# Performance work log

Measured on AMD Instinct MI355X. Metric: run time of the kernel, lower is better.

The kernel has to match this reference:

```python
import jax, jax.numpy as jnp
import numpy as np

NH = 16   # num_heads
HD = 128  # head_dim
HS = 2048 # hidden_size
LI, LT = 2048, 512
MLP = 4 * HS


def _ln(x, s, b):
    m = jnp.mean(x, axis=-1, keepdims=True)
    v = jnp.var(x, axis=-1, keepdims=True)
    return (x - m) * jax.lax.rsqrt(v + 1e-6) * s + b


def _rms(x, s):
    return x * jax.lax.rsqrt(jnp.mean(x * x, axis=-1, keepdims=True) + 1e-6) * s


def _mod6(vec, w, b):
    a = (jax.nn.silu(vec) @ w + b)[:, None, :]
    return jnp.split(a, 6, axis=-1)  # shift1,scale1,gate1,shift2,scale2,gate2


def _rope(x, pe):
    B, H, L, D = x.shape
    xr = x.reshape(B, H, L, D // 2, 1, 2)
    return (pe[..., 0] * xr[..., 0] + pe[..., 1] * xr[..., 1]).reshape(B, H, L, D)


def _attention(q, k, v, pe):
    q = _rope(q, pe)
    k = _rope(k, pe)
    scores = jnp.einsum('bhqd,bhkd->bhqk', q, k) * (q.shape[-1] ** -0.5)
    p = jax.nn.softmax(scores, axis=-1)
    o = jnp.einsum('bhqk,bhkd->bhqd', p, v)
    B, H, L, D = o.shape
    return o.transpose(0, 2, 1, 3).reshape(B, L, H * D)


def _prenorm_qkv(x, shift, scale, ln_s, ln_b, qkv_w, qkv_b, qn, kn):
    xm = (1.0 + scale) * _ln(x, ln_s, ln_b) + shift
    y = xm @ qkv_w + qkv_b
    B, L, _ = y.shape
    y = y.reshape(B, L, 3, NH, HD).transpose(2, 0, 3, 1, 4)  # K B H L D
    q, k, v = y[0], y[1], y[2]
    return _rms(q, qn), _rms(k, kn), v


def _forward(img, txt, vec, pe,
             img_mod_w, img_mod_b, img_norm1_s, img_norm1_b, img_qkv_w, img_qkv_b,
             img_qn_s, img_kn_s, img_proj_w, img_proj_b, img_norm2_s, img_norm2_b,
             img_mlp_w1, img_mlp_b1, img_mlp_w2, img_mlp_b2,
             txt_mod_w, txt_mod_b, txt_norm1_s, txt_norm1_b, txt_qkv_w, txt_qkv_b,
             txt_qn_s, txt_kn_s, txt_proj_w, txt_proj_b, txt_norm2_s, txt_norm2_b,
             txt_mlp_w1, txt_mlp_b1, txt_mlp_w2, txt_mlp_b2):
    i_sh1, i_sc1, i_g1, i_sh2, i_sc2, i_g2 = _mod6(vec, img_mod_w, img_mod_b)
    t_sh1, t_sc1, t_g1, t_sh2, t_sc2, t_g2 = _mod6(vec, txt_mod_w, txt_mod_b)

    iq, ik, iv = _prenorm_qkv(img, i_sh1, i_sc1, img_norm1_s, img_norm1_b,
                              img_qkv_w, img_qkv_b, img_qn_s, img_kn_s)
    tq, tk, tv = _prenorm_qkv(txt, t_sh1, t_sc1, txt_norm1_s, txt_norm1_b,
                              txt_qkv_w, txt_qkv_b, txt_qn_s, txt_kn_s)

    q = jnp.concatenate((tq, iq), axis=2)
    k = jnp.concatenate((tk, ik), axis=2)
    v = jnp.concatenate((tv, iv), axis=2)
    attn = _attention(q, k, v, pe)  # [B, LT+LI, HS]
    Lt = txt.shape[1]
    txt_attn, img_attn = attn[:, :Lt], attn[:, Lt:]

    img = img + i_g1 * (img_attn @ img_proj_w + img_proj_b)
    img_h = (1.0 + i_sc2) * _ln(img, img_norm2_s, img_norm2_b) + i_sh2
    img = img + i_g2 * (jax.nn.gelu(img_h @ img_mlp_w1 + img_mlp_b1) @ img_mlp_w2 + img_mlp_b2)

    txt = txt + t_g1 * (txt_attn @ txt_proj_w + txt_proj_b)
    txt_h = (1.0 + t_sc2) * _ln(txt, txt_norm2_s, txt_norm2_b) + t_sh2
    txt = txt + t_g2 * (jax.nn.gelu(txt_h @ txt_mlp_w1 + txt_mlp_b1) @ txt_mlp_w2 + txt_mlp_b2)
    return img, txt


def setup_inputs() -> dict:
    key = jax.random.key(0)
    ki = iter(jax.random.split(key, 48))
    def n(shape, s=0.02):
        return jax.random.normal(next(ki), shape, jnp.float32) * s
    d = {
        'img': jax.random.normal(next(ki), (1, LI, HS), jnp.float32),
        'txt': jax.random.normal(next(ki), (1, LT, HS), jnp.float32),
        'vec': jax.random.normal(next(ki), (1, HS), jnp.float32),
        'pe': jax.random.normal(next(ki), (1, 1, LT + LI, HD // 2, 2, 2), jnp.float32),
    }
    for p in ('img', 'txt'):
        d[p + '_mod_w'] = n((HS, 6 * HS)); d[p + '_mod_b'] = jnp.zeros((6 * HS,), jnp.float32)
        d[p + '_norm1_s'] = jnp.ones((HS,), jnp.float32); d[p + '_norm1_b'] = jnp.zeros((HS,), jnp.float32)
        d[p + '_qkv_w'] = n((HS, 3 * HS)); d[p + '_qkv_b'] = jnp.zeros((3 * HS,), jnp.float32)
        d[p + '_qn_s'] = jnp.ones((HD,), jnp.float32); d[p + '_kn_s'] = jnp.ones((HD,), jnp.float32)
        d[p + '_proj_w'] = n((HS, HS)); d[p + '_proj_b'] = jnp.zeros((HS,), jnp.float32)
        d[p + '_norm2_s'] = jnp.ones((HS,), jnp.float32); d[p + '_norm2_b'] = jnp.zeros((HS,), jnp.float32)
        d[p + '_mlp_w1'] = n((HS, MLP)); d[p + '_mlp_b1'] = jnp.zeros((MLP,), jnp.float32)
        d[p + '_mlp_w2'] = n((MLP, HS)); d[p + '_mlp_b2'] = jnp.zeros((HS,), jnp.float32)
    return d


def reference(img, txt, vec, pe,
              img_mod_w, img_mod_b, img_norm1_s, img_norm1_b, img_qkv_w, img_qkv_b,
              img_qn_s, img_kn_s, img_proj_w, img_proj_b, img_norm2_s, img_norm2_b,
              img_mlp_w1, img_mlp_b1, img_mlp_w2, img_mlp_b2,
              txt_mod_w, txt_mod_b, txt_norm1_s, txt_norm1_b, txt_qkv_w, txt_qkv_b,
              txt_qn_s, txt_kn_s, txt_proj_w, txt_proj_b, txt_norm2_s, txt_norm2_b,
              txt_mlp_w1, txt_mlp_b1, txt_mlp_w2, txt_mlp_b2):
    return _forward(img, txt, vec, pe,
                    img_mod_w, img_mod_b, img_norm1_s, img_norm1_b, img_qkv_w, img_qkv_b,
                    img_qn_s, img_kn_s, img_proj_w, img_proj_b, img_norm2_s, img_norm2_b,
                    img_mlp_w1, img_mlp_b1, img_mlp_w2, img_mlp_b2,
                    txt_mod_w, txt_mod_b, txt_norm1_s, txt_norm1_b, txt_qkv_w, txt_qkv_b,
                    txt_qn_s, txt_kn_s, txt_proj_w, txt_proj_b, txt_norm2_s, txt_norm2_b,
                    txt_mlp_w1, txt_mlp_b1, txt_mlp_w2, txt_mlp_b2)
```

## Files before the change

### kernel.cpp

```cpp
#include <hip/hip_runtime.h>
#include <hip/hip_bf16.h>
#include <math.h>

typedef __bf16 bf16;
typedef __bf16 bf16x2 __attribute__((ext_vector_type(2)));
typedef __bf16 bf16x8 __attribute__((ext_vector_type(8)));
typedef float f32x4 __attribute__((ext_vector_type(4)));

#define HS 2048
#define NH 16
#define HD 128
#define LT 512
#define LI 2048
#define LQ 2560
#define MLP_D 8192
#define SPLIT 4
#define KVS (LQ / SPLIT)
#define KVBLK 32
#define NTILES (KVS / KVBLK)

__device__ __forceinline__ f32x4 mfma16(bf16x8 a, bf16x8 b, f32x4 c) {
  return __builtin_amdgcn_mfma_f32_16x16x32_bf16(a, b, c, 0, 0, 0);
}

__device__ __forceinline__ void gl_lds16(const bf16* g, bf16* l) {
  __builtin_amdgcn_global_load_lds((const __attribute__((address_space(1))) void*)g,
                                   (__attribute__((address_space(3))) void*)l, 16, 0, 0);
}

__global__ void k_silu(const float* __restrict__ v, float* __restrict__ s) {
  int i = blockIdx.x * 256 + threadIdx.x;
  float x = v[i];
  s[i] = x / (1.f + expf(-x));
}

__global__ __launch_bounds__(256) void k_mod_partial(
    const float* __restrict__ s, const float* __restrict__ w_txt,
    const float* __restrict__ w_img, float* __restrict__ part) {
  int strm = blockIdx.x / 48;
  int n = (blockIdx.x % 48) * 256 + threadIdx.x;
  const float* w = strm ? w_img : w_txt;
  int k0 = blockIdx.y * 256;
  __shared__ float sl[256];
  sl[threadIdx.x] = s[k0 + threadIdx.x];
  __syncthreads();
  float acc = 0.f;
  for (int k = 0; k < 256; k++)
    acc += sl[k] * w[(size_t)(k0 + k) * 12288 + n];
  part[((size_t)blockIdx.y * 2 + strm) * 12288 + n] = acc;
}

__global__ __launch_bounds__(256) void k_mod_reduce(
    const float* __restrict__ part, const float* __restrict__ b_txt,
    const float* __restrict__ b_img, float* __restrict__ mod) {
  int strm = blockIdx.x / 48;
  int n = (blockIdx.x % 48) * 256 + threadIdx.x;
  float acc = strm ? b_img[n] : b_txt[n];
  for (int kc = 0; kc < 8; kc++)
    acc += part[((size_t)kc * 2 + strm) * 12288 + n];
  mod[(size_t)strm * 12288 + n] = acc;
}

__global__ __launch_bounds__(256) void k_transpose_cvt(
    const float* __restrict__ src, bf16* __restrict__ dst, int R, int C) {
  __shared__ float t[64][65];
  int tx = threadIdx.x & 63, ty = threadIdx.x >> 6;
  int c0 = blockIdx.x * 64, r0 = blockIdx.y * 64;
  for (int i = 0; i < 64; i += 4)
    t[ty + i][tx] = src[(size_t)(r0 + ty + i) * C + c0 + tx];
  __syncthreads();
#pragma unroll
  for (int j = 0; j < 2; j++) {
    int c = (threadIdx.x >> 3) + j * 32;
    int gg = (threadIdx.x & 7) * 8;
    bf16x8 ov;
#pragma unroll
    for (int k = 0; k < 8; k++) ov[k] = (bf16)t[gg + k][c];
    *(bf16x8*)(dst + (size_t)(c0 + c) * R + r0 + gg) = ov;
  }
}

__global__ __launch_bounds__(256) void k_ln_mod(
    const float* __restrict__ x0, const float* __restrict__ x1,
    const float* __restrict__ ls0, const float* __restrict__ lb0,
    const float* __restrict__ ls1, const float* __restrict__ lb1,
    const float* __restrict__ mod0, const float* __restrict__ mod1,
    int shidx, int scidx, bf16* __restrict__ out) {
  int r = blockIdx.x;
  int strm = r >= LT;
  const float* x = strm ? (x1 + (size_t)(r - LT) * HS) : (x0 + (size_t)r * HS);
  const float* ls = strm ? ls1 : ls0;
  const float* lb = strm ? lb1 : lb0;
  const float* md = strm ? mod1 : mod0;
  const float* sh = md + (size_t)shidx * HS;
  const float* sc = md + (size_t)scidx * HS;
  int t = threadIdx.x;
  float4 a = ((const float4*)x)[t * 2];
  float4 b = ((const float4*)x)[t * 2 + 1];
  float xv[8] = {a.x, a.y, a.z, a.w, b.x, b.y, b.z, b.w};
  float sum = 0.f, sq = 0.f;
#pragma unroll
  for (int j = 0; j < 8; j++) { sum += xv[j]; sq += xv[j] * xv[j]; }
#pragma unroll
  for (int m = 32; m; m >>= 1) { sum += __shfl_xor(sum, m); sq += __shfl_xor(sq, m); }
  __shared__ float red[8];
  int lane = t & 63, wid = t >> 6;
  if (!lane) { red[wid] = sum; red[wid + 4] = sq; }
  __syncthreads();
  float ts = red[0] + red[1] + red[2] + red[3];
  float tq = red[4] + red[5] + red[6] + red[7];
  float mean = ts * (1.f / HS);
  float var = tq * (1.f / HS) - mean * mean;
  float inv = rsqrtf(var + 1e-6f);
  int c0 = t * 8;
  bf16x8 ov;
#pragma unroll
  for (int j = 0; j < 8; j++) {
    int c = c0 + j;
    float v = ((xv[j] - mean) * inv * ls[c] + lb[c]) * (1.f + sc[c]) + sh[c];
    ov[j] = (bf16)v;
  }
  *(bf16x8*)(out + (size_t)r * HS + c0) = ov;
}

template <int MODE>
__global__ __launch_bounds__(256) void k_gemm(
    const bf16* __restrict__ A, int K, int N, int Ksz,
    const bf16* __restrict__ BT0, const bf16* __restrict__ BT1,
    const float* __restrict__ bias0, const float* __restrict__ bias1,
    void* __restrict__ out0, void* __restrict__ out1) {
  __shared__ bf16 As[128 * 32];
  __shared__ bf16 Bs[128 * 32];
  int tid = threadIdx.x;
  int bn = blockIdx.x, bm = blockIdx.y;
  int strm = (bm * 128) >= LT;
  int lm = bm * 128 - strm * LT;
  const bf16* BT = strm ? BT1 : BT0;
  int lane = tid & 63, wid = tid >> 6;
  int wr = wid >> 1, wc = wid & 1;
  int sr = tid >> 2, sc8 = (tid & 3) * 8;
  const bf16* Ag = A + (size_t)(bm * 128 + sr) * K + sc8;
  const bf16* Bg = BT + (size_t)(bn * 128 + sr) * K + sc8;
  bf16* As_dst = As + wid * 512;
  bf16* Bs_dst = Bs + wid * 512;
  int kbeg = MODE == 4 ? blockIdx.z * Ksz : 0;
  f32x4 acc[4][4] = {};
  for (int k0 = kbeg; k0 < kbeg + Ksz; k0 += 32) {
    __syncthreads();
    gl_lds16(Ag + k0, As_dst);
    gl_lds16(Ag + (size_t)64 * K + k0, As_dst + 2048);
    gl_lds16(Bg + k0, Bs_dst);
    gl_lds16(Bg + (size_t)64 * K + k0, Bs_dst + 2048);
    __syncthreads();
    bf16x8 af[4], bfr[4];
    int r16 = lane & 15, kc8 = (lane >> 4) * 8;
#pragma unroll
    for (int m = 0; m < 4; m++) af[m] = *(const bf16x8*)&As[(wr * 64 + m * 16 + r16) * 32 + kc8];
#pragma unroll
    for (int n = 0; n < 4; n++) bfr[n] = *(const bf16x8*)&Bs[(wc * 64 + n * 16 + r16) * 32 + kc8];
#pragma unroll
    for (int m = 0; m < 4; m++)
#pragma unroll
      for (int n = 0; n < 4; n++)
        acc[m][n] = mfma16(af[m], bfr[n], acc[m][n]);
  }
  int col = lane & 15, rb = (lane >> 4) * 4;
  const float* bias = strm ? bias1 : bias0;
  float* part = MODE == 4 ? (float*)out0 + (size_t)blockIdx.z * LQ * N : nullptr;
#pragma unroll
  for (int m = 0; m < 4; m++) {
#pragma unroll
    for (int n = 0; n < 4; n++) {
      int gn = bn * 128 + wc * 64 + n * 16 + col;
      float bv = MODE == 4 ? 0.f : bias[gn];
#pragma unroll
      for (int r = 0; r < 4; r++) {
        int lr = wr * 64 + m * 16 + rb + r;
        float v = acc[m][n][r] + bv;
        if (MODE == 0) {
          ((bf16*)(strm ? out1 : out0))[(size_t)(lm + lr) * N + gn] = (bf16)v;
        } else if (MODE == 2) {
          float g = 0.5f * v * (1.f + tanhf(0.7978845608028654f * (v + 0.044715f * v * v * v)));
          ((bf16*)(strm ? out1 : out0))[(size_t)(lm + lr) * N + gn] = (bf16)g;
        } else {
          part[(size_t)(bm * 128 + lr) * N + gn] = v;
        }
      }
    }
  }
}

template <int S>
__global__ __launch_bounds__(256) void k_skcomb(
    const float* __restrict__ part, int N,
    const float* __restrict__ bias0, const float* __restrict__ bias1,
    const float* __restrict__ gate0, const float* __restrict__ gate1,
    const float* __restrict__ res0, const float* __restrict__ res1,
    float* __restrict__ out0, float* __restrict__ out1) {
  int gid = blockIdx.x * 256 + threadIdx.x;
  int nv = N >> 2;
  int row = gid / nv, cv = gid - row * nv;
  int strm = row >= LT;
  int lrow = row - strm * LT;
  const float* bias = strm ? bias1 : bias0;
  const float* gate = strm ? gate1 : gate0;
  const float* res = strm ? res1 : res0;
  float* out = strm ? out1 : out0;
  int c = cv * 4;
  float4 acc = *(const float4*)(bias + c);
#pragma unroll
  for (int s = 0; s < S; s++) {
    float4 p = *(const float4*)(part + ((size_t)s * LQ + row) * N + c);
    acc.x += p.x; acc.y += p.y; acc.z += p.z; acc.w += p.w;
  }
  float4 g = *(const float4*)(gate + c);
  float4 r = *(const float4*)(res + (size_t)lrow * N + c);
  float4 o = {r.x + g.x * acc.x, r.y + g.y * acc.y, r.z + g.z * acc.z, r.w + g.w * acc.w};
  *(float4*)(out + (size_t)lrow * N + c) = o;
}

__global__ __launch_bounds__(256) void k_qkv_post(
    const bf16* __restrict__ y, const float* __restrict__ pe,
    const float* __restrict__ qn0, const float* __restrict__ kn0,
    const float* __restrict__ qn1, const float* __restrict__ kn1,
    bf16* __restrict__ qh, bf16* __restrict__ kh) {
  int wv = (int)((blockIdx.x * 256 + threadIdx.x) >> 6);
  int lane = threadIdx.x & 63;
  int head = wv / LQ, l = wv - head * LQ;
  const bf16* yr = y + (size_t)l * (3 * HS) + head * HD;
  float q0 = (float)yr[2 * lane], q1 = (float)yr[2 * lane + 1];
  float k0 = (float)yr[HS + 2 * lane], k1 = (float)yr[HS + 2 * lane + 1];
  float sqs = q0 * q0 + q1 * q1, sks = k0 * k0 + k1 * k1;
#pragma unroll
  for (int m = 1; m < 64; m <<= 1) { sqs += __shfl_xor(sqs, m); sks += __shfl_xor(sks, m); }
  float rq = rsqrtf(sqs * (1.f / HD) + 1e-6f);
  float rk = rsqrtf(sks * (1.f / HD) + 1e-6f);
  int strm = l >= LT;
  const float* qn = strm ? qn1 : qn0;
  const float* kn = strm ? kn1 : kn0;
  float e0 = q0 * rq * qn[2 * lane], e1 = q1 * rq * qn[2 * lane + 1];
  float f0 = k0 * rk * kn[2 * lane], f1 = k1 * rk * kn[2 * lane + 1];
  float4 p = *(const float4*)(pe + ((size_t)l * 64 + lane) * 4);
  const float scl = 0.08838834764831845f;
  size_t qi = ((size_t)head * LQ + l) * HD + 2 * lane;
  bf16x2 qv = {(bf16)((p.x * e0 + p.y * e1) * scl), (bf16)((p.z * e0 + p.w * e1) * scl)};
  bf16x2 kv = {(bf16)(p.x * f0 + p.y * f1), (bf16)(p.z * f0 + p.w * f1)};
  *(bf16x2*)(qh + qi) = qv;
  *(bf16x2*)(kh + qi) = kv;
}

__global__ __launch_bounds__(256) void k_vtrans(const bf16* __restrict__ y,
                                                bf16* __restrict__ vT) {
  __shared__ bf16 t[32][34];
  int head = blockIdx.y >> 2, dt = blockIdx.y & 3;
  int tx = threadIdx.x & 31, ty = threadIdx.x >> 5;
  int l0 = blockIdx.x * 32, d0 = dt * 32;
  for (int i = 0; i < 32; i += 8)
    t[ty + i][tx] = y[(size_t)(l0 + ty + i) * (3 * HS) + 2 * HS + head * HD + d0 + tx];
  __syncthreads();
  for (int i = 0; i < 32; i += 8)
    vT[(size_t)(head * HD + d0 + ty + i) * LQ + l0 + tx] = t[tx][ty + i];
}

__global__ __launch_bounds__(256, 4) void k_attn(
    const bf16* __restrict__ Q, const bf16* __restrict__ Kh,
    const bf16* __restrict__ VT, bf16* __restrict__ Op, float* __restrict__ ml) {
  __shared__ bf16 Ks[2][KVBLK * 128];
  __shared__ bf16 Vs[2][128 * KVBLK];
  __shared__ bf16 P[4][16 * 34];
  int tid = threadIdx.x, lane = tid & 63, w = tid >> 6;
  int b = blockIdx.x;
  int qb = b % 40;
  int split = (b / 40) % SPLIT;
  int head = b / (40 * SPLIT);
  int qr = qb * 64 + w * 16;
  int r16 = lane & 15, g = lane >> 4;
  const bf16* qp = Q + ((size_t)head * LQ + qr + r16) * HD + g * 8;
  bf16x8 qf[4];
#pragma unroll
  for (int c = 0; c < 4; c++) qf[c] = *(const bf16x8*)(qp + c * 32);
  f32x4 O[8] = {};
  float mr[4], lr[4];
#pragma unroll
  for (int i = 0; i < 4; i++) { mr[i] = -1e30f; lr[i] = 0.f; }
  bf16* pl = &P[w][0];
  const bf16* kbase = Kh + ((size_t)head * LQ + split * KVS) * HD;
  const bf16* vbase = VT + (size_t)head * HD * LQ + split * KVS;
  int krow0 = w * 8 + (lane >> 4);
  int kslot = lane & 15;
  int vrow0 = w * 32 + (lane >> 2);
  int vslot = lane & 3;
  auto stage = [&](int buf, int t) {
    int kv0 = t * KVBLK;
#pragma unroll
    for (int i = 0; i < 2; i++) {
      int krow = krow0 + i * 4;
      gl_lds16(kbase + (size_t)(kv0 + krow) * HD + ((kslot ^ (krow & 7)) << 3),
               &Ks[buf][(w * 8 + i * 4) * 128]);
      int vrow = vrow0 + i * 16;
      gl_lds16(vbase + (size_t)vrow * LQ + kv0 + ((vslot ^ (vrow & 3)) << 3),
               &Vs[buf][(w * 32 + i * 16) * KVBLK]);
    }
  };
  stage(0, 0);
  int cur = 0;
  for (int t = 0; t < NTILES; t++) {
    __syncthreads();
    if (t + 1 < NTILES) stage(cur ^ 1, t + 1);
    const bf16* ks = &Ks[cur][0];
    const bf16* vs = &Vs[cur][0];
    f32x4 S0 = {}, S1 = {};
    int sw = (r16 & 7);
#pragma unroll
    for (int c = 0; c < 4; c++) {
      int slot = ((4 * c + g) ^ sw) << 3;
      bf16x8 ka = *(const bf16x8*)&ks[r16 * 128 + slot];
      bf16x8 kb = *(const bf16x8*)&ks[(16 + r16) * 128 + slot];
      S0 = mfma16(qf[c], ka, S0);
      S1 = mfma16(qf[c], kb, S1);
    }
    float alpha[4];
#pragma unroll
    for (int i = 0; i < 4; i++) {
      float mx = fmaxf(S0[i], S1[i]);
#pragma unroll
      for (int m = 8; m; m >>= 1) mx = fmaxf(mx, __shfl_xor(mx, m));
      float mn = fmaxf(mr[i], mx);
      float p0 = __expf(S0[i] - mn), p1 = __expf(S1[i] - mn);
      float rs = p0 + p1;
#pragma unroll
      for (int m = 8; m; m >>= 1) rs += __shfl_xor(rs, m);
      alpha[i] = __expf(mr[i] - mn);
      lr[i] = lr[i] * alpha[i] + rs;
      mr[i] = mn;
      pl[(4 * g + i) * 34 + r16] = (bf16)p0;
      pl[(4 * g + i) * 34 + 16 + r16] = (bf16)p1;
    }
    bf16x8 pf = *(const bf16x8*)&pl[r16 * 34 + g * 8];
    int vsl = (g ^ (r16 & 3)) * 8;
#pragma unroll
    for (int n = 0; n < 8; n++) {
      f32x4 o = O[n];
#pragma unroll
      for (int i = 0; i < 4; i++) o[i] *= alpha[i];
      bf16x8 vf = *(const bf16x8*)&vs[(n * 16 + r16) * KVBLK + vsl];
      O[n] = mfma16(pf, vf, o);
    }
    cur ^= 1;
  }
  const int NL = NH * LQ;
  bf16* op = Op + (size_t)split * NL * HD;
#pragma unroll
  for (int n = 0; n < 8; n++)
#pragma unroll
    for (int i = 0; i < 4; i++)
      op[((size_t)head * LQ + qr + 4 * g + i) * HD + n * 16 + r16] = (bf16)O[n][i];
  if (r16 == 0) {
#pragma unroll
    for (int i = 0; i < 4; i++) {
      int idx = head * LQ + qr + 4 * g + i;
      ml[(size_t)(split * 2 + 0) * NL + idx] = mr[i];
      ml[(size_t)(split * 2 + 1) * NL + idx] = lr[i];
    }
  }
}

__global__ __launch_bounds__(256) void k_attn_combine(
    const bf16* __restrict__ Op, const float* __restrict__ ml, bf16* __restrict__ out) {
  int lane = threadIdx.x & 63, w = threadIdx.x >> 6;
  int row = blockIdx.x * 4 + w;
  int head = row / LQ, l = row - head * LQ;
  const int NL = NH * LQ;
  float ms[SPLIT], ls[SPLIT], m = -1e30f;
#pragma unroll
  for (int s = 0; s < SPLIT; s++) {
    ms[s] = ml[(size_t)(s * 2) * NL + row];
    ls[s] = ml[(size_t)(s * 2 + 1) * NL + row];
    m = fmaxf(m, ms[s]);
  }
  float wsum = 0.f, wgt[SPLIT];
#pragma unroll
  for (int s = 0; s < SPLIT; s++) { wgt[s] = __expf(ms[s] - m); wsum += wgt[s] * ls[s]; }
  float inv = 1.f / wsum;
  size_t oi = (size_t)row * HD + 2 * lane;
  float a0 = 0.f, a1 = 0.f;
#pragma unroll
  for (int s = 0; s < SPLIT; s++) {
    bf16x2 v = *(const bf16x2*)(Op + (size_t)s * NL * HD + oi);
    a0 += wgt[s] * (float)v[0];
    a1 += wgt[s] * (float)v[1];
  }
  bf16x2 ov = {(bf16)(a0 * inv), (bf16)(a1 * inv)};
  *(bf16x2*)(out + (size_t)l * HS + head * HD + 2 * lane) = ov;
}

extern "C" void kernel_launch(void* const* d_in, const int* in_sizes, int n_in,
                              void* d_out, int out_size, void* d_ws, size_t ws_size,
                              hipStream_t stream) {
  const float* img = (const float*)d_in[0];
  const float* txt = (const float*)d_in[1];
  const float* vec = (const float*)d_in[2];
  const float* pe = (const float*)d_in[3];
#define PARAM(i) ((const float*)d_in[i])

  char* ws = (char*)d_ws;
  size_t off = 0;
  auto alloc = [&](size_t b) { void* p = ws + off; off += (b + 255) & ~(size_t)255; return p; };
  float* silu_s = (float*)alloc((size_t)HS * 4);
  float* mpart = (float*)alloc((size_t)8 * 2 * 12288 * 4);
  float* mod = (float*)alloc((size_t)2 * 6 * HS * 4);
  bf16* qkvT0 = (bf16*)alloc((size_t)3 * HS * HS * 2);
  bf16* qkvT1 = (bf16*)alloc((size_t)3 * HS * HS * 2);
  bf16* projT0 = (bf16*)alloc((size_t)HS * HS * 2);
  bf16* projT1 = (bf16*)alloc((size_t)HS * HS * 2);
  bf16* mlp1T0 = (bf16*)alloc((size_t)MLP_D * HS * 2);
  bf16* mlp1T1 = (bf16*)alloc((size_t)MLP_D * HS * 2);
  bf16* mlp2T0 = (bf16*)alloc((size_t)HS * MLP_D * 2);
  bf16* mlp2T1 = (bf16*)alloc((size_t)HS * MLP_D * 2);
  bf16* xm = (bf16*)alloc((size_t)LQ * HS * 2);
  bf16* y = (bf16*)alloc((size_t)LQ * 3 * HS * 2);
  bf16* qh = (bf16*)alloc((size_t)NH * LQ * HD * 2);
  bf16* kh = (bf16*)alloc((size_t)NH * LQ * HD * 2);
  bf16* vT = (bf16*)alloc((size_t)NH * HD * LQ * 2);
  bf16* attnb = (bf16*)alloc((size_t)LQ * HS * 2);
  float* x2 = (float*)alloc((size_t)LQ * HS * 4);
  bf16* xm2 = (bf16*)alloc((size_t)LQ * HS * 2);
  bf16* h = (bf16*)alloc((size_t)LQ * MLP_D * 2);
  float* ml = (float*)alloc((size_t)2 * SPLIT * NH * LQ * 4);
  bf16* Op = h;
  float* skpart = (float*)xm;
  (void)ws_size; (void)in_sizes; (void)n_in; (void)out_size;

  const float* t_mod = mod;
  const float* i_mod = mod + 6 * HS;

  k_silu<<<HS / 256, 256, 0, stream>>>(vec, silu_s);
  k_mod_partial<<<dim3(96, 8), 256, 0, stream>>>(silu_s, PARAM(20), PARAM(4), mpart);
  k_mod_reduce<<<96, 256, 0, stream>>>(mpart, PARAM(21), PARAM(5), mod);

  k_transpose_cvt<<<dim3(3 * HS / 64, HS / 64), 256, 0, stream>>>(PARAM(24), qkvT0, HS, 3 * HS);
  k_transpose_cvt<<<dim3(3 * HS / 64, HS / 64), 256, 0, stream>>>(PARAM(8), qkvT1, HS, 3 * HS);
  k_transpose_cvt<<<dim3(HS / 64, HS / 64), 256, 0, stream>>>(PARAM(28), projT0, HS, HS);
  k_transpose_cvt<<<dim3(HS / 64, HS / 64), 256, 0, stream>>>(PARAM(12), projT1, HS, HS);
  k_transpose_cvt<<<dim3(MLP_D / 64, HS / 64), 256, 0, stream>>>(PARAM(32), mlp1T0, HS, MLP_D);
  k_transpose_cvt<<<dim3(MLP_D / 64, HS / 64), 256, 0, stream>>>(PARAM(16), mlp1T1, HS, MLP_D);
  k_transpose_cvt<<<dim3(HS / 64, MLP_D / 64), 256, 0, stream>>>(PARAM(34), mlp2T0, MLP_D, HS);
  k_transpose_cvt<<<dim3(HS / 64, MLP_D / 64), 256, 0, stream>>>(PARAM(18), mlp2T1, MLP_D, HS);

  k_ln_mod<<<LQ, 256, 0, stream>>>(txt, img, PARAM(22), PARAM(23), PARAM(6), PARAM(7),
                                   t_mod, i_mod, 0, 1, xm);

  k_gemm<0><<<dim3(3 * HS / 128, LQ / 128), 256, 0, stream>>>(
      xm, HS, 3 * HS, HS, qkvT0, qkvT1, PARAM(25), PARAM(9), y, y + (size_t)LT * 3 * HS);

  k_qkv_post<<<NH * LQ / 4, 256, 0, stream>>>(y, pe, PARAM(26), PARAM(27), PARAM(10), PARAM(11),
                                              qh, kh);
  k_vtrans<<<dim3(LQ / 32, NH * 4), 256, 0, stream>>>(y, vT);

  k_attn<<<NH * SPLIT * 40, 256, 0, stream>>>(qh, kh, vT, Op, ml);
  k_attn_combine<<<NH * LQ / 4, 256, 0, stream>>>(Op, ml, attnb);

  k_gemm<4><<<dim3(HS / 128, LQ / 128, 2), 256, 0, stream>>>(
      attnb, HS, HS, HS / 2, projT0, projT1, nullptr, nullptr, skpart, nullptr);
  k_skcomb<2><<<LQ * HS / 4 / 256, 256, 0, stream>>>(
      skpart, HS, PARAM(29), PARAM(13), t_mod + 2 * HS, i_mod + 2 * HS, txt, img,
      x2, x2 + (size_t)LT * HS);

  k_ln_mod<<<LQ, 256, 0, stream>>>(x2, x2 + (size_t)LT * HS, PARAM(30), PARAM(31), PARAM(14),
                                   PARAM(15), t_mod, i_mod, 3, 4, xm2);

  k_gemm<2><<<dim3(MLP_D / 128, LQ / 128), 256, 0, stream>>>(
      xm2, HS, MLP_D, HS, mlp1T0, mlp1T1, PARAM(33), PARAM(17), h, h + (size_t)LT * MLP_D);

  float* out_img = (float*)d_out;
  float* out_txt = (float*)d_out + (size_t)LI * HS;
  k_gemm<4><<<dim3(HS / 128, LQ / 128, 4), 256, 0, stream>>>(
      h, MLP_D, HS, MLP_D / 4, mlp2T0, mlp2T1, nullptr, nullptr, skpart, nullptr);
  k_skcomb<4><<<LQ * HS / 4 / 256, 256, 0, stream>>>(
      skpart, HS, PARAM(35), PARAM(19), t_mod + 5 * HS, i_mod + 5 * HS, x2,
      x2 + (size_t)LT * HS, out_txt, out_img);
}
```

Before: 860.4 us.

## Double-buffer GEMM LDS tiles, XOR-swizzle shared layout, use exp-based GELU

```diff
diff --git a/kernel.cpp b/kernel.cpp
--- a/kernel.cpp
+++ b/kernel.cpp
@@ -129,8 +129,8 @@
     const bf16* __restrict__ BT0, const bf16* __restrict__ BT1,
     const float* __restrict__ bias0, const float* __restrict__ bias1,
     void* __restrict__ out0, void* __restrict__ out1) {
-  __shared__ bf16 As[128 * 32];
-  __shared__ bf16 Bs[128 * 32];
+  __shared__ bf16 As[2][128 * 32];
+  __shared__ bf16 Bs[2][128 * 32];
   int tid = threadIdx.x;
   int bn = blockIdx.x, bm = blockIdx.y;
   int strm = (bm * 128) >= LT;
@@ -138,31 +138,40 @@
   const bf16* BT = strm ? BT1 : BT0;
   int lane = tid & 63, wid = tid >> 6;
   int wr = wid >> 1, wc = wid & 1;
-  int sr = tid >> 2, sc8 = (tid & 3) * 8;
-  const bf16* Ag = A + (size_t)(bm * 128 + sr) * K + sc8;
-  const bf16* Bg = BT + (size_t)(bn * 128 + sr) * K + sc8;
-  bf16* As_dst = As + wid * 512;
-  bf16* Bs_dst = Bs + wid * 512;
+  int sr = tid >> 2;
+  int scol = ((tid & 3) ^ (sr & 3)) * 8;
+  const bf16* Ag = A + (size_t)(bm * 128 + sr) * K + scol;
+  const bf16* Bg = BT + (size_t)(bn * 128 + sr) * K + scol;
   int kbeg = MODE == 4 ? blockIdx.z * Ksz : 0;
+  int nk = Ksz / 32;
+  auto stage = [&](int buf, int ks) {
+    int k0 = kbeg + ks * 32;
+    gl_lds16(Ag + k0, &As[buf][wid * 512]);
+    gl_lds16(Ag + (size_t)64 * K + k0, &As[buf][2048 + wid * 512]);
+    gl_lds16(Bg + k0, &Bs[buf][wid * 512]);
+    gl_lds16(Bg + (size_t)64 * K + k0, &Bs[buf][2048 + wid * 512]);
+  };
   f32x4 acc[4][4] = {};
-  for (int k0 = kbeg; k0 < kbeg + Ksz; k0 += 32) {
+  int r16 = lane & 15, g = lane >> 4;
+  int fslot = (g ^ (r16 & 3)) * 8;
+  stage(0, 0);
+  int cur = 0;
+  for (int ks = 0; ks < nk; ks++) {
     __syncthreads();
-    gl_lds16(Ag + k0, As_dst);
-    gl_lds16(Ag + (size_t)64 * K + k0, As_dst + 2048);
-    gl_lds16(Bg + k0, Bs_dst);
-    gl_lds16(Bg + (size_t)64 * K + k0, Bs_dst + 2048);
-    __syncthreads();
+    if (ks + 1 < nk) stage(cur ^ 1, ks + 1);
     bf16x8 af[4], bfr[4];
-    int r16 = lane & 15, kc8 = (lane >> 4) * 8;
-#pragma unroll
-    for (int m = 0; m < 4; m++) af[m] = *(const bf16x8*)&As[(wr * 64 + m * 16 + r16) * 32 + kc8];
-#pragma unroll
-    for (int n = 0; n < 4; n++) bfr[n] = *(const bf16x8*)&Bs[(wc * 64 + n * 16 + r16) * 32 + kc8];
+#pragma unroll
+    for (int m = 0; m < 4; m++)
+      af[m] = *(const bf16x8*)&As[cur][(wr * 64 + m * 16 + r16) * 32 + fslot];
+#pragma unroll
+    for (int n = 0; n < 4; n++)
+      bfr[n] = *(const bf16x8*)&Bs[cur][(wc * 64 + n * 16 + r16) * 32 + fslot];
 #pragma unroll
     for (int m = 0; m < 4; m++)
 #pragma unroll
       for (int n = 0; n < 4; n++)
         acc[m][n] = mfma16(af[m], bfr[n], acc[m][n]);
+    cur ^= 1;
   }
   int col = lane & 15, rb = (lane >> 4) * 4;
   const float* bias = strm ? bias1 : bias0;
@@ -180,8 +189,9 @@
         if (MODE == 0) {
           ((bf16*)(strm ? out1 : out0))[(size_t)(lm + lr) * N + gn] = (bf16)v;
         } else if (MODE == 2) {
-          float g = 0.5f * v * (1.f + tanhf(0.7978845608028654f * (v + 0.044715f * v * v * v)));
-          ((bf16*)(strm ? out1 : out0))[(size_t)(lm + lr) * N + gn] = (bf16)g;
+          float u2 = 1.5957691216057308f * (v + 0.044715f * v * v * v);
+          float ge = v / (1.f + __expf(-u2));
+          ((bf16*)(strm ? out1 : out0))[(size_t)(lm + lr) * N + gn] = (bf16)ge;
         } else {
           part[(size_t)(bm * 128 + lr) * N + gn] = v;
         }
```

Result: faster. 822.8 us (-4.4%).
